# Kernel tuning notes

Measured on AMD Instinct MI355X. Metric: run time of the kernel, lower is better.

Reference implementation:

```python
import jax, jax.numpy as jnp
import numpy as np
from jax import lax

B0, H0, W0, C0, NH0 = 8, 128, 128, 192, 6
SPLIT = (8, 16)
BN_EPS = 1e-5


def setup_inputs() -> dict:
    key = jax.random.key(0)
    ks = jax.random.split(key, 32)
    r = lambda i, shape, s=0.02: jax.random.normal(ks[i], shape, dtype=jnp.float32) * s
    C, C8 = C0, C0 // 8
    L = H0 * W0
    return dict(
        x=jax.random.normal(ks[0], (B0, L, C), dtype=jnp.float32),
        w_qkv=r(1, (C, 3 * C)), b_qkv=r(2, (3 * C,)),
        w_dw1=r(3, (C, 1, 3, 3), 0.1), b_dw1=r(4, (C,)),
        g_bn1=1.0 + r(5, (C,)), be_bn1=r(6, (C,)),
        w_si1=r(7, (C8, C), 0.05), b_si1=r(8, (C8,)),
        g_si=1.0 + r(9, (C8,)), be_si=r(10, (C8,)),
        w_si2=r(11, (1, C8), 0.05), b_si2=r(12, (1,)),
        w_ci1=r(13, (C8, C), 0.05), b_ci1=r(14, (C8,)),
        g_ci=1.0 + r(15, (C8,)), be_ci=r(16, (C8,)),
        w_ci2=r(17, (C, C8), 0.05), b_ci2=r(18, (C,)),
        w_dw2=r(19, (C, 1, 3, 3), 0.1), b_dw2=r(20, (C,)),
        g_bn2=1.0 + r(21, (C,)), be_bn2=r(22, (C,)),
        w_proj=r(23, (C, C)), b_proj=r(24, (C,)),
        H=H0, W=W0,
    )


def _bn(x, g, b):  # eval-mode BatchNorm2d, running_mean=0, running_var=1, NCHW
    return x * (g / jnp.sqrt(1.0 + BN_EPS))[:, None, None] + b[:, None, None]


def _gelu(x):
    return jax.nn.gelu(x, approximate=False)  # torch nn.GELU default (erf)


def _dwconv3x3(x, w, b):  # x:(B,C,H,W), w:(C,1,3,3) depthwise
    y = lax.conv_general_dilated(x, w, (1, 1), 'SAME',
                                 feature_group_count=x.shape[1],
                                 dimension_numbers=('NCHW', 'OIHW', 'NCHW'))
    return y + b[:, None, None]


def _c1x1(x, w, b):  # 1x1 conv, w:(O,C)
    return jnp.einsum('bchw,oc->bohw', x, w) + b[:, None, None]


def _win_attn(q, k, v, H, W, Hs, Ws, nh):
    # q,k,v: (B, H*W, Cb). qkv1==qkv2==qkv3 in the source (same Linear on same x),
    # so attn1+attn2+attn3 == 3*attn1 and v1+v2+v3 == 3*v1 (faithful math).
    B, L, Cb = q.shape
    hd = Cb // nh
    scale = hd ** (-0.5)
    T = Hs * Ws

    def to_win(t):  # (B,L,Cb) -> (nW, nh, T, hd)
        t = t.reshape(B, H // Hs, Hs, W // Ws, Ws, Cb)
        t = t.transpose(0, 1, 3, 2, 4, 5).reshape(-1, T, nh, hd)
        return t.transpose(0, 2, 1, 3)

    qw, kw, vw = to_win(q), to_win(k), to_win(v)
    attn = jnp.einsum('wntd,wnsd->wnts', qw, kw) * (3.0 * scale)
    attn = jax.nn.softmax(attn, axis=-1)
    out = jnp.einsum('wnts,wnsd->wntd', attn, 3.0 * vw)  # (nW, nh, T, hd)
    out = out.transpose(0, 2, 1, 3).reshape(-1, T, Cb)
    out = out.reshape(B, H // Hs, W // Ws, Hs, Ws, Cb)
    out = out.transpose(0, 1, 3, 2, 4, 5).reshape(B, H, W, Cb)
    return out


def _forward(x, w_qkv, b_qkv, w_dw1, b_dw1, g_bn1, be_bn1,
             w_si1, b_si1, g_si, be_si, w_si2, b_si2,
             w_ci1, b_ci1, g_ci, be_ci, w_ci2, b_ci2,
             w_dw2, b_dw2, g_bn2, be_bn2, w_proj, b_proj, H, W):
    B, L, C = x.shape
    Ch = C // 2
    nh = NH0 // 2

    qkv = (x @ w_qkv + b_qkv).reshape(B, L, 3, C).transpose(2, 0, 1, 3)  # (3,B,L,C)
    mx = max(SPLIT)
    pad_b = (mx - H % mx) % mx
    pad_r = (mx - W % mx) % mx
    qi = qkv.reshape(3 * B, H, W, C)
    qi = jnp.pad(qi, ((0, 0), (0, pad_b), (0, pad_r), (0, 0)))
    _H, _W = H + pad_b, W + pad_r
    qkv = qi.reshape(3, B, _H * _W, C)
    q, k, v = qkv[0], qkv[1], qkv[2]

    fu1 = _win_attn(q[..., :Ch], k[..., :Ch], v[..., :Ch], _H, _W, SPLIT[0], SPLIT[1], nh)
    fu2 = _win_attn(q[..., Ch:], k[..., Ch:], v[..., Ch:], _H, _W, SPLIT[1], SPLIT[0], nh)
    fu = jnp.concatenate([fu1[:, :H, :W, :].reshape(B, L, Ch),
                          fu2[:, :H, :W, :].reshape(B, L, Ch)], axis=-1)

    # NOTE: the source does x.reshape(B,C,L) (a raw reshape, NOT a transpose) -- replicated.
    x_img = x.reshape(B, C, H, W)
    conv_x1 = _gelu(_bn(_dwconv3x3(x_img, w_dw1, b_dw1), g_bn1, be_bn1))

    s = _c1x1(conv_x1, w_si1, b_si1)
    s = _c1x1(_gelu(_bn(s, g_si, be_si)), w_si2, b_si2)   # (B,1,H,W)
    spatial_map = s.reshape(B, L, 1)

    c = conv_x1.mean(axis=(2, 3), keepdims=True)           # AdaptiveAvgPool2d(1)
    c = _c1x1(c, w_ci1, b_ci1)
    c = _c1x1(_gelu(_bn(c, g_ci, be_ci)), w_ci2, b_ci2)    # (B,C,1,1)
    channel_map = c.reshape(B, 1, C)

    fu = fu + fu * jax.nn.sigmoid(spatial_map)
    fu_img = jnp.swapaxes(fu, -2, -1).reshape(B, C, H, W)
    fu_img = _gelu(_bn(_dwconv3x3(fu_img, w_dw2, b_dw2), g_bn2, be_bn2))
    fu = fu_img.transpose(0, 2, 3, 1).reshape(B, L, C)
    fu = fu + fu * jax.nn.sigmoid(channel_map)
    return fu @ w_proj + b_proj


def reference(x, w_qkv, b_qkv, w_dw1, b_dw1, g_bn1, be_bn1,
              w_si1, b_si1, g_si, be_si, w_si2, b_si2,
              w_ci1, b_ci1, g_ci, be_ci, w_ci2, b_ci2,
              w_dw2, b_dw2, g_bn2, be_bn2, w_proj, b_proj, H, W):
    return _forward(x, w_qkv, b_qkv, w_dw1, b_dw1, g_bn1, be_bn1,
                    w_si1, b_si1, g_si, be_si, w_si2, b_si2,
                    w_ci1, b_ci1, g_ci, be_ci, w_ci2, b_ci2,
                    w_dw2, b_dw2, g_bn2, be_bn2, w_proj, b_proj, H, W)
```

## Files before the change

### kernel.cpp

```cpp
#include <hip/hip_runtime.h>

#define Bn 8
#define Hn 128
#define Wn 128
#define Cn 192
#define Ln (Hn*Wn)
#define Mn (Bn*Ln)
#define FUn ((size_t)Mn*Cn)
#define BANKn ((size_t)Mn*96)
#define BN_RSQ 0.9999950000374997f

typedef unsigned short ushort_t;
typedef __attribute__((ext_vector_type(8))) short short8;
typedef __attribute__((ext_vector_type(4))) float f32x4;
typedef __attribute__((ext_vector_type(4))) unsigned int uint4v;

static __device__ __forceinline__ float gelu_f(float x) {
    return 0.5f * x * (1.0f + erff(x * 0.7071067811865475f));
}
static __device__ __forceinline__ float gate1p(float x) {
    return 1.0f + 1.0f / (1.0f + __expf(-x));
}
static __device__ __forceinline__ unsigned short f2bf(float f) {
    unsigned u = __float_as_uint(f);
    return (unsigned short)((u + 0x7FFFu + ((u >> 16) & 1u)) >> 16);
}
static __device__ __forceinline__ unsigned int pk2(float lo, float hi) {
    return (unsigned int)f2bf(lo) | ((unsigned int)f2bf(hi) << 16);
}
static __device__ __forceinline__ float bf2f(ushort_t u) {
    return __uint_as_float((unsigned)u << 16);
}

__global__ __launch_bounds__(256) void qkv_mfma(const ushort_t* __restrict__ Ab,
        const float* __restrict__ Bw, const float* __restrict__ bias,
        ushort_t* __restrict__ Qp, ushort_t* __restrict__ Kp,
        ushort_t* __restrict__ Vp)
{
    __shared__ __align__(16) ushort_t As[128 * 64];
    __shared__ __align__(16) ushort_t Bs[96 * 64];
    const int m0 = blockIdx.y * 128;
    const int n0g = blockIdx.x * 96;
    const int part = n0g / 192;
    const int coln = n0g - part * 192;
    ushort_t* dst = part == 0 ? Qp : (part == 1 ? Kp : Vp);
    ushort_t* bptr = dst + (coln ? BANKn : 0);
    const int tid = threadIdx.x;
    const int lane = tid & 63;
    const int wrow = (tid >> 6) * 32;
    const int r0 = lane >> 4, cl = lane & 15;
    f32x4 acc[2][6] = {};

    for (int ks = 0; ks < 3; ++ks) {
        const int k0 = ks * 64;
        if (ks) __syncthreads();
        #pragma unroll
        for (int i = 0; i < 2; ++i) {
            int s = tid + i * 256;
            int row = s >> 2, q = s & 3;
            const ushort_t* src = Ab + (size_t)(m0 + row) * 192 + k0 + q * 16;
            uint4 u0 = *(const uint4*)(src);
            uint4 u1 = *(const uint4*)(src + 8);
            int r7 = row & 7;
            *(uint4*)&As[row * 64 + (((q * 2) ^ r7) * 8)] = u0;
            *(uint4*)&As[row * 64 + (((q * 2 + 1) ^ r7) * 8)] = u1;
        }
        #pragma unroll
        for (int i = 0; i < 3; ++i) {
            int f = tid + i * 256;
            int col = f % 96, kslot = f / 96;
            uint4v wv;
            #pragma unroll
            for (int e2 = 0; e2 < 4; ++e2) {
                float lo = Bw[(size_t)(k0 + kslot * 8 + 2 * e2)     * 576 + n0g + col];
                float hi = Bw[(size_t)(k0 + kslot * 8 + 2 * e2 + 1) * 576 + n0g + col];
                wv[e2] = pk2(lo, hi);
            }
            *(uint4v*)&Bs[col * 64 + ((kslot ^ (col & 7)) * 8)] = wv;
        }
        __syncthreads();
        #pragma unroll
        for (int kk = 0; kk < 2; ++kk) {
            int kslot = kk * 4 + r0;
            int ra0 = wrow + cl, ra1 = wrow + 16 + cl;
            short8 a0 = *(const short8*)&As[ra0 * 64 + ((kslot ^ (ra0 & 7)) * 8)];
            short8 a1 = *(const short8*)&As[ra1 * 64 + ((kslot ^ (ra1 & 7)) * 8)];
            #pragma unroll
            for (int n = 0; n < 6; ++n) {
                int col = n * 16 + cl;
                short8 bn = *(const short8*)&Bs[col * 64 + ((kslot ^ (col & 7)) * 8)];
                acc[0][n] = __builtin_amdgcn_mfma_f32_16x16x32_bf16(a0, bn, acc[0][n], 0, 0, 0);
                acc[1][n] = __builtin_amdgcn_mfma_f32_16x16x32_bf16(a1, bn, acc[1][n], 0, 0, 0);
            }
        }
    }
    float bv[6];
    #pragma unroll
    for (int n = 0; n < 6; ++n) bv[n] = bias[n0g + n * 16 + cl];
    #pragma unroll
    for (int m = 0; m < 2; ++m) {
        #pragma unroll
        for (int j = 0; j < 4; ++j) {
            int row = m0 + wrow + m * 16 + r0 * 4 + j;
            int b = row >> 14, l = row & 16383;
            int h = l >> 7, w = l & 127;
            int win, t;
            if (coln == 0) { win = (h >> 3) * 8 + (w >> 4);  t = (h & 7) * 16 + (w & 15); }
            else           { win = (h >> 4) * 16 + (w >> 3); t = (h & 15) * 8 + (w & 7); }
            size_t rbase = ((size_t)((b * 128 + win) * 128 + t)) * 96;
            #pragma unroll
            for (int n = 0; n < 6; ++n)
                bptr[rbase + n * 16 + cl] = f2bf(acc[m][n][j] + bv[n]);
        }
    }
}

__global__ __launch_bounds__(256) void proj_mfma(const ushort_t* __restrict__ Ab,
        const float* __restrict__ Bw, const float* __restrict__ bias,
        float* __restrict__ Cout)
{
    __shared__ __align__(16) ushort_t As[128 * 64];
    __shared__ __align__(16) ushort_t Bs[96 * 64];
    const int m0 = blockIdx.x * 128;
    const int n0 = blockIdx.y * 96;
    const int tid = threadIdx.x;
    const int lane = tid & 63;
    const int wrow = (tid >> 6) * 32;
    const int r0 = lane >> 4, cl = lane & 15;
    f32x4 acc[2][6] = {};

    for (int ks = 0; ks < 3; ++ks) {
        const int k0 = ks * 64;
        if (ks) __syncthreads();
        #pragma unroll
        for (int i = 0; i < 2; ++i) {
            int s = tid + i * 256;
            int row = s >> 2, q = s & 3;
            const ushort_t* src = Ab + (size_t)(m0 + row) * 192 + k0 + q * 16;
            uint4 u0 = *(const uint4*)(src);
            uint4 u1 = *(const uint4*)(src + 8);
            int r7 = row & 7;
            *(uint4*)&As[row * 64 + (((q * 2) ^ r7) * 8)] = u0;
            *(uint4*)&As[row * 64 + (((q * 2 + 1) ^ r7) * 8)] = u1;
        }
        #pragma unroll
        for (int i = 0; i < 3; ++i) {
            int f = tid + i * 256;
            int col = f % 96, kslot = f / 96;
            uint4v wv;
            #pragma unroll
            for (int e2 = 0; e2 < 4; ++e2) {
                float lo = Bw[(size_t)(k0 + kslot * 8 + 2 * e2)     * 192 + n0 + col];
                float hi = Bw[(size_t)(k0 + kslot * 8 + 2 * e2 + 1) * 192 + n0 + col];
                wv[e2] = pk2(lo, hi);
            }
            *(uint4v*)&Bs[col * 64 + ((kslot ^ (col & 7)) * 8)] = wv;
        }
        __syncthreads();
        #pragma unroll
        for (int kk = 0; kk < 2; ++kk) {
            int kslot = kk * 4 + r0;
            int ra0 = wrow + cl, ra1 = wrow + 16 + cl;
            short8 a0 = *(const short8*)&As[ra0 * 64 + ((kslot ^ (ra0 & 7)) * 8)];
            short8 a1 = *(const short8*)&As[ra1 * 64 + ((kslot ^ (ra1 & 7)) * 8)];
            #pragma unroll
            for (int n = 0; n < 6; ++n) {
                int col = n * 16 + cl;
                short8 bn = *(const short8*)&Bs[col * 64 + ((kslot ^ (col & 7)) * 8)];
                acc[0][n] = __builtin_amdgcn_mfma_f32_16x16x32_bf16(a0, bn, acc[0][n], 0, 0, 0);
                acc[1][n] = __builtin_amdgcn_mfma_f32_16x16x32_bf16(a1, bn, acc[1][n], 0, 0, 0);
            }
        }
    }
    #pragma unroll
    for (int m = 0; m < 2; ++m) {
        #pragma unroll
        for (int n = 0; n < 6; ++n) {
            int col = n0 + n * 16 + cl;
            float bv = bias[col];
            #pragma unroll
            for (int j = 0; j < 4; ++j) {
                int row = m0 + wrow + m * 16 + r0 * 4 + j;
                Cout[(size_t)row * 192 + col] = acc[m][n][j] + bv;
            }
        }
    }
}

__global__ __launch_bounds__(256) void attn_mfma(const ushort_t* __restrict__ Qp,
        const ushort_t* __restrict__ Kp, const ushort_t* __restrict__ Vp,
        const float* __restrict__ gate_s, ushort_t* __restrict__ fu_b)
{
    const int widx = threadIdx.x >> 6;
    const int idx = blockIdx.x * 4 + widx;
    const int jhalf = idx & 1;
    const int sub0 = idx >> 1;
    const int branch = (sub0 >= 3072) ? 1 : 0;
    const int sub = sub0 - branch * 3072;
    const int head = sub >> 10;
    const int b = (sub >> 7) & 7;
    const int win = sub & 127;
    const int L = threadIdx.x & 63;
    const int g = L >> 4, q = L & 15;
    int hb, wb;
    if (branch == 0) { hb = (win >> 3) * 8;  wb = (win & 7) * 16; }
    else             { hb = (win >> 4) * 16; wb = (win & 15) * 8; }
    const int cf = branch * 96 + head * 32;
    const int hch = head * 32;
    const int jbase = jhalf * 4;

    const size_t bank = branch ? BANKn : 0;
    const size_t wbase = ((size_t)((b * 128 + win) * 128)) * 96;
    const ushort_t* Qw = Qp + bank + wbase;
    const ushort_t* Kw = Kp + bank + wbase;
    const ushort_t* Vw = Vp + bank + wbase;

    short8 kf[8], qf[4];
    #pragma unroll
    for (int i = 0; i < 8; ++i)
        kf[i] = *(const short8*)(Kw + (size_t)(16 * i + q) * 96 + hch + 8 * g);
    #pragma unroll
    for (int jj = 0; jj < 4; ++jj)
        qf[jj] = *(const short8*)(Qw + (size_t)(16 * (jbase + jj) + q) * 96 + hch + 8 * g);
    short8 vf[2][4];
    {
        #pragma unroll
        for (int s = 0; s < 4; ++s) {
            #pragma unroll
            for (int dblk = 0; dblk < 2; ++dblk) {
                uint4v wv;
                #pragma unroll
                for (int e2 = 0; e2 < 4; ++e2) {
                    size_t base = (size_t)(32 * s + 8 * g + 2 * e2) * 96 + hch + 16 * dblk + q;
                    unsigned lo = Vw[base];
                    unsigned hi = Vw[base + 96];
                    wv[e2] = lo | (hi << 16);
                }
                vf[dblk][s] = *(short8*)&wv;
            }
        }
    }

    const float SC = 0.5303300858899106f;
    const int src0 = q + ((g & 1) << 5);
    const bool thi = (g >> 1) != 0;
    const bool glo = (g < 2);
    #pragma unroll
    for (int jj = 0; jj < 4; ++jj) {
        const int j = jbase + jj;
        unsigned wA[8], wB[8];
        float ss = 0.0f;
        #pragma unroll
        for (int i = 0; i < 8; ++i) {
            f32x4 z = {};
            f32x4 S = __builtin_amdgcn_mfma_f32_16x16x32_bf16(kf[i], qf[jj], z, 0, 0, 0);
            float p0 = __expf(S[0] * SC), p1 = __expf(S[1] * SC);
            float p2 = __expf(S[2] * SC), p3 = __expf(S[3] * SC);
            ss += (p0 + p1) + (p2 + p3);
            wA[i] = pk2(p0, p1);
            wB[i] = pk2(p2, p3);
        }
        ss += __shfl_xor(ss, 16);
        ss += __shfl_xor(ss, 32);
        int l_own;
        if (branch == 0) l_own = (hb + j) * Wn + wb + q;
        else             l_own = (hb + 2 * j + (q >> 3)) * Wn + wb + (q & 7);
        float s_own = 3.0f * gate_s[(size_t)b * Ln + l_own] / ss;

        f32x4 O0 = {}, O1 = {};
        #pragma unroll
        for (int s = 0; s < 4; ++s) {
            unsigned a0  = (unsigned)__shfl((int)wA[2*s],     src0);
            unsigned b0  = (unsigned)__shfl((int)wB[2*s],     src0);
            unsigned a0h = (unsigned)__shfl((int)wA[2*s],     src0 + 16);
            unsigned b0h = (unsigned)__shfl((int)wB[2*s],     src0 + 16);
            unsigned a1  = (unsigned)__shfl((int)wA[2*s+1],   src0);
            unsigned b1  = (unsigned)__shfl((int)wB[2*s+1],   src0);
            unsigned a1h = (unsigned)__shfl((int)wA[2*s+1],   src0 + 16);
            unsigned b1h = (unsigned)__shfl((int)wB[2*s+1],   src0 + 16);
            uint4v B2u;
            B2u[0] = thi ? a1  : a0;
            B2u[1] = thi ? b1  : b0;
            B2u[2] = thi ? a1h : a0h;
            B2u[3] = thi ? b1h : b0h;
            short8 B2 = *(short8*)&B2u;
            O0 = __builtin_amdgcn_mfma_f32_16x16x32_bf16(vf[0][s], B2, O0, 0, 0, 0);
            O1 = __builtin_amdgcn_mfma_f32_16x16x32_bf16(vf[1][s], B2, O1, 0, 0, 0);
        }
        unsigned w0 = pk2(O0[0] * s_own, O0[1] * s_own);
        unsigned w1 = pk2(O0[2] * s_own, O0[3] * s_own);
        unsigned w2 = pk2(O1[0] * s_own, O1[1] * s_own);
        unsigned w3 = pk2(O1[2] * s_own, O1[3] * s_own);
        unsigned a0 = (unsigned)__shfl((int)w0, src0);
        unsigned a1 = (unsigned)__shfl((int)w1, src0);
        unsigned b0 = (unsigned)__shfl((int)w0, src0 + 16);
        unsigned b1 = (unsigned)__shfl((int)w1, src0 + 16);
        unsigned c0 = (unsigned)__shfl((int)w2, src0);
        unsigned c1 = (unsigned)__shfl((int)w3, src0);
        unsigned d0 = (unsigned)__shfl((int)w2, src0 + 16);
        unsigned d1 = (unsigned)__shfl((int)w3, src0 + 16);
        uint4 o = make_uint4(glo ? a0 : c0, glo ? a1 : c1,
                             glo ? b0 : d0, glo ? b1 : d1);
        *(uint4*)(fu_b + (size_t)(b * Ln + l_own) * 192 + cf + 8 * g) = o;
    }
}

__global__ __launch_bounds__(256) void conv1_k(const float* __restrict__ x,
        const float* __restrict__ wdw, const float* __restrict__ bdw,
        const float* __restrict__ g1, const float* __restrict__ be1,
        ushort_t* __restrict__ conv1b, ushort_t* __restrict__ xb,
        float* __restrict__ pooled2)
{
    int bc = blockIdx.x;
    int half = blockIdx.y;
    int c = bc % 192;
    const float* plane = x + (size_t)bc * Ln;
    ushort_t* oplane = conv1b + (size_t)bc * Ln;
    ushort_t* xplane = xb + (size_t)bc * Ln;
    int t = threadIdx.x;
    int sx = t & 31, sy = t >> 5;
    int w0 = sx * 4, h0 = half * 64 + sy * 8;
    float wk[9];
    #pragma unroll
    for (int i = 0; i < 9; ++i) wk[i] = wdw[c * 9 + i];
    float gb = g1[c] * BN_RSQ, bb = be1[c], bd = bdw[c];

    float r[10][6];
    #pragma unroll
    for (int i = 0; i < 10; ++i) {
        int h = h0 - 1 + i;
        float4 m = make_float4(0.f, 0.f, 0.f, 0.f);
        if (h >= 0 && h < Hn)
            m = *(const float4*)(plane + h * Wn + w0);
        float lf = __shfl_up(m.w, 1);
        float rt = __shfl_down(m.x, 1);
        r[i][0] = sx ? lf : 0.0f;
        r[i][1] = m.x; r[i][2] = m.y; r[i][3] = m.z; r[i][4] = m.w;
        r[i][5] = (sx < 31) ? rt : 0.0f;
    }
    float psum = 0.0f;
    #pragma unroll
    for (int i = 0; i < 8; ++i) {
        int h = h0 + i;
        *(uint2*)(xplane + h * Wn + w0) =
            make_uint2(pk2(r[i+1][1], r[i+1][2]), pk2(r[i+1][3], r[i+1][4]));
        float o[4];
        #pragma unroll
        for (int p = 0; p < 4; ++p) {
            float s = wk[0] * r[i][p];
            s = fmaf(wk[1], r[i][p + 1], s);
            s = fmaf(wk[2], r[i][p + 2], s);
            s = fmaf(wk[3], r[i+1][p],     s);
            s = fmaf(wk[4], r[i+1][p + 1], s);
            s = fmaf(wk[5], r[i+1][p + 2], s);
            s = fmaf(wk[6], r[i+2][p],     s);
            s = fmaf(wk[7], r[i+2][p + 1], s);
            s = fmaf(wk[8], r[i+2][p + 2], s);
            float y = gelu_f((s + bd) * gb + bb);
            psum += y;
            o[p] = y;
        }
        *(uint2*)(oplane + h * Wn + w0) =
            make_uint2(pk2(o[0], o[1]), pk2(o[2], o[3]));
    }
    __shared__ float red[4];
    for (int off = 32; off; off >>= 1) psum += __shfl_down(psum, off);
    if ((t & 63) == 0) red[t >> 6] = psum;
    __syncthreads();
    if (t == 0)
        pooled2[bc * 2 + half] = red[0] + red[1] + red[2] + red[3];
}

__global__ __launch_bounds__(128) void spatial_gate_k(const ushort_t* __restrict__ conv1b,
        const float* __restrict__ ws1g, const float* __restrict__ bs1,
        const float* __restrict__ gsi, const float* __restrict__ besi,
        const float* __restrict__ ws2, const float* __restrict__ bs2,
        float* __restrict__ gate_s)
{
    int bh = blockIdx.x;
    int b = bh >> 7, h = bh & 127;
    int w = threadIdx.x;
    __shared__ float ws1T[192 * 24];
    for (int i = w; i < 192 * 24; i += 128) {
        int c = i / 24, o = i - c * 24;
        ws1T[i] = ws1g[o * 192 + c];
    }
    __syncthreads();
    float acc24[24] = {};
    const ushort_t* base = conv1b + (size_t)b * 192 * Ln + h * Wn + w;
    #pragma unroll 4
    for (int c = 0; c < 192; ++c) {
        float v = bf2f(base[(size_t)c * Ln]);
        const float4* wp = (const float4*)&ws1T[c * 24];
        #pragma unroll
        for (int o4 = 0; o4 < 6; ++o4) {
            float4 wv = wp[o4];
            acc24[o4*4+0] = fmaf(v, wv.x, acc24[o4*4+0]);
            acc24[o4*4+1] = fmaf(v, wv.y, acc24[o4*4+1]);
            acc24[o4*4+2] = fmaf(v, wv.z, acc24[o4*4+2]);
            acc24[o4*4+3] = fmaf(v, wv.w, acc24[o4*4+3]);
        }
    }
    float s2 = bs2[0];
    #pragma unroll
    for (int o = 0; o < 24; ++o)
        s2 = fmaf(gelu_f((acc24[o] + bs1[o]) * (gsi[o] * BN_RSQ) + besi[o]), ws2[o], s2);
    gate_s[(size_t)bh * 128 + w] = gate1p(s2);
}

__global__ __launch_bounds__(192) void channel_gate_k(const float* __restrict__ pooled2,
        const float* __restrict__ w1, const float* __restrict__ b1,
        const float* __restrict__ g, const float* __restrict__ be,
        const float* __restrict__ w2, const float* __restrict__ b2,
        float* __restrict__ gate_c)
{
    int b = blockIdx.x, t = threadIdx.x;
    __shared__ float pl[192];
    __shared__ float h1[24];
    int bc = b * 192 + t;
    pl[t] = (pooled2[bc * 2] + pooled2[bc * 2 + 1]) * (1.0f / Ln);
    __syncthreads();
    if (t < 24) {
        float a = b1[t];
        for (int c = 0; c < 192; ++c) a = fmaf(pl[c], w1[t * 192 + c], a);
        a = a * (g[t] * BN_RSQ) + be[t];
        h1[t] = gelu_f(a);
    }
    __syncthreads();
    float a = b2[t];
    #pragma unroll
    for (int o = 0; o < 24; ++o) a = fmaf(h1[o], w2[t * 24 + o], a);
    gate_c[b * 192 + t] = gate1p(a);
}

__global__ __launch_bounds__(256) void dwconv2_k(const ushort_t* __restrict__ fu_b,
        const float* __restrict__ gate_c,
        const float* __restrict__ wdw, const float* __restrict__ bdw,
        const float* __restrict__ g2, const float* __restrict__ be2,
        ushort_t* __restrict__ out2b)
{
    int bh = blockIdx.x >> 1;
    int whalf = blockIdx.x & 1;
    int b = bh >> 7, h = bh & 127;
    int tid = threadIdx.x;
    __shared__ float cwp[24 * 105];
    for (int idx = tid; idx < 24 * 96; idx += 256) {
        int c8 = idx / 96, r = idx - c8 * 96;
        float v;
        if (r < 72) {
            int i = r / 9, p = r - i * 9;
            v = wdw[(c8 * 8 + i) * 9 + p];
        } else {
            int r2 = r - 72;
            int i = r2 / 3, j = r2 - i * 3;
            int c = c8 * 8 + i;
            float A = g2[c] * BN_RSQ;
            v = (j == 0) ? A : (j == 1) ? fmaf(bdw[c], A, be2[c])
                                        : gate_c[b * 192 + c];
        }
        cwp[c8 * 105 + r] = v;
    }
    __syncthreads();
    const size_t outrow = (size_t)(b * Ln + h * Wn) * 192;
    for (int it = 0; it < 6; ++it) {
        int item = it * 256 + tid;
        int w = whalf * 64 + item / 24;
        int c8 = item % 24;
        int co = c8 * 8;
        const float* wp = &cwp[c8 * 105];
        uint4 nb[3][3];
        #pragma unroll
        for (int r = 0; r < 3; ++r)
            #pragma unroll
            for (int d = 0; d < 3; ++d)
                nb[r][d] = make_uint4(0u, 0u, 0u, 0u);
        #pragma unroll
        for (int r = 0; r < 3; ++r) {
            int hh = h - 1 + r;
            if (hh < 0 || hh >= Hn) continue;
            const ushort_t* rp = fu_b + (size_t)(b * Ln + hh * Wn) * 192 + co;
            #pragma unroll
            for (int d = 0; d < 3; ++d) {
                int w2 = w - 1 + d;
                if (w2 < 0 || w2 >= Wn) continue;
                nb[r][d] = *(const uint4*)(rp + (size_t)w2 * 192);
            }
        }
        unsigned ou[4];
        #pragma unroll
        for (int i = 0; i < 8; ++i) {
            float s = 0.0f;
            #pragma unroll
            for (int r = 0; r < 3; ++r) {
                #pragma unroll
                for (int d = 0; d < 3; ++d) {
                    unsigned word = ((const unsigned*)&nb[r][d])[i >> 1];
                    float v = __uint_as_float((i & 1) ? (word & 0xffff0000u)
                                                      : (word << 16));
                    s = fmaf(wp[i * 9 + r * 3 + d], v, s);
                }
            }
            float A = wp[72 + i * 3];
            float Bc = wp[72 + i * 3 + 1];
            float G = wp[72 + i * 3 + 2];
            float y = gelu_f(fmaf(s, A, Bc)) * G;
            if (i & 1) ou[i >> 1] |= (unsigned)f2bf(y) << 16;
            else       ou[i >> 1] = (unsigned)f2bf(y);
        }
        *(uint4*)(out2b + outrow + (size_t)w * 192 + co) =
            make_uint4(ou[0], ou[1], ou[2], ou[3]);
    }
}

extern "C" void kernel_launch(void* const* d_in, const int* in_sizes, int n_in,
                              void* d_out, int out_size, void* d_ws, size_t ws_size,
                              hipStream_t stream) {
    (void)in_sizes; (void)n_in; (void)out_size; (void)ws_size;
    const float* x      = (const float*)d_in[0];
    const float* w_qkv  = (const float*)d_in[1];
    const float* b_qkv  = (const float*)d_in[2];
    const float* w_dw1  = (const float*)d_in[3];
    const float* b_dw1  = (const float*)d_in[4];
    const float* g_bn1  = (const float*)d_in[5];
    const float* be_bn1 = (const float*)d_in[6];
    const float* w_si1  = (const float*)d_in[7];
    const float* b_si1  = (const float*)d_in[8];
    const float* g_si   = (const float*)d_in[9];
    const float* be_si  = (const float*)d_in[10];
    const float* w_si2  = (const float*)d_in[11];
    const float* b_si2  = (const float*)d_in[12];
    const float* w_ci1  = (const float*)d_in[13];
    const float* b_ci1  = (const float*)d_in[14];
    const float* g_ci   = (const float*)d_in[15];
    const float* be_ci  = (const float*)d_in[16];
    const float* w_ci2  = (const float*)d_in[17];
    const float* b_ci2  = (const float*)d_in[18];
    const float* w_dw2  = (const float*)d_in[19];
    const float* b_dw2  = (const float*)d_in[20];
    const float* g_bn2  = (const float*)d_in[21];
    const float* be_bn2 = (const float*)d_in[22];
    const float* w_proj = (const float*)d_in[23];
    const float* b_proj = (const float*)d_in[24];

    float* ws = (float*)d_ws;
    ushort_t* conv1b = (ushort_t*)ws;
    ushort_t* Qp     = (ushort_t*)ws;
    ushort_t* Kp     = (ushort_t*)(ws + FUn / 2);
    ushort_t* out2b  = (ushort_t*)(ws + 8000000);
    float* gate_s    = ws + FUn;
    float* gate_c    = gate_s + (size_t)Bn * Ln;
    float* pooled2   = gate_c + Bn * 192;
    ushort_t* xb     = (ushort_t*)d_out;
    ushort_t* fu_b   = (ushort_t*)d_out;
    ushort_t* Vp     = (ushort_t*)d_out + FUn;

    conv1_k<<<dim3(Bn * 192, 2), 256, 0, stream>>>(x, w_dw1, b_dw1, g_bn1, be_bn1,
                                                   conv1b, xb, pooled2);
    spatial_gate_k<<<Bn * Hn, 128, 0, stream>>>(conv1b, w_si1, b_si1, g_si, be_si,
                                                w_si2, b_si2, gate_s);
    channel_gate_k<<<Bn, 192, 0, stream>>>(pooled2, w_ci1, b_ci1, g_ci, be_ci,
                                           w_ci2, b_ci2, gate_c);
    qkv_mfma<<<dim3(6, Mn / 128), 256, 0, stream>>>(xb, w_qkv, b_qkv, Qp, Kp, Vp);
    attn_mfma<<<3072, 256, 0, stream>>>(Qp, Kp, Vp, gate_s, fu_b);
    dwconv2_k<<<Bn * Hn * 2, 256, 0, stream>>>(fu_b, gate_c,
                                               w_dw2, b_dw2, g_bn2, be_bn2, out2b);
    proj_mfma<<<dim3(Mn / 128, 2), 256, 0, stream>>>(out2b, w_proj, b_proj, (float*)d_out);
}
```

Baseline: 310.5 us.

## Store Q/K/V per-head contiguous with transposed V; split conv1 into more blocks

The QKV GEMM epilogue now writes each window/head as a contiguous 128x32 tile, with V stored transposed (channel-major), so the attention kernel loads K, Q and V fragments as vector short8 loads instead of strided scalar gathers. Separately, conv1 is split into 16 row groups per plane, one row per thread, so it launches more blocks and reloads fewer halo rows per thread, with 16 partial pooled sums reduced in channel_gate. The scattered 2-byte epilogue stores in the QKV kernel may become less coalesced, and conv1 re-reads two halo rows per output row.

```diff
diff --git a/kernel.cpp b/kernel.cpp
--- a/kernel.cpp
+++ b/kernel.cpp
@@ -107,10 +107,15 @@
             int win, t;
             if (coln == 0) { win = (h >> 3) * 8 + (w >> 4);  t = (h & 7) * 16 + (w & 15); }
             else           { win = (h >> 4) * 16 + (w >> 3); t = (h & 15) * 8 + (w & 7); }
-            size_t rbase = ((size_t)((b * 128 + win) * 128 + t)) * 96;
-            #pragma unroll
-            for (int n = 0; n < 6; ++n)
-                bptr[rbase + n * 16 + cl] = f2bf(acc[m][n][j] + bv[n]);
+            size_t wb3 = (size_t)(b * 128 + win) * 3;
+            #pragma unroll
+            for (int n = 0; n < 6; ++n) {
+                int col96 = n * 16 + cl;
+                int head = col96 >> 5, ch = col96 & 31;
+                size_t off = (wb3 + head) * 4096 +
+                             (part == 2 ? ch * 128 + t : t * 32 + ch);
+                bptr[off] = f2bf(acc[m][n][j] + bv[n]);
+            }
         }
     }
 }
@@ -206,40 +211,27 @@
     if (branch == 0) { hb = (win >> 3) * 8;  wb = (win & 7) * 16; }
     else             { hb = (win >> 4) * 16; wb = (win & 15) * 8; }
     const int cf = branch * 96 + head * 32;
-    const int hch = head * 32;
     const int jbase = jhalf * 4;
 
-    const size_t bank = branch ? BANKn : 0;
-    const size_t wbase = ((size_t)((b * 128 + win) * 128)) * 96;
-    const ushort_t* Qw = Qp + bank + wbase;
-    const ushort_t* Kw = Kp + bank + wbase;
-    const ushort_t* Vw = Vp + bank + wbase;
+    const size_t base = (branch ? BANKn : 0)
+                      + ((size_t)(b * 128 + win) * 3 + head) * 4096;
+    const ushort_t* Qw = Qp + base;
+    const ushort_t* Kw = Kp + base;
+    const ushort_t* Vw = Vp + base;
 
     short8 kf[8], qf[4];
     #pragma unroll
     for (int i = 0; i < 8; ++i)
-        kf[i] = *(const short8*)(Kw + (size_t)(16 * i + q) * 96 + hch + 8 * g);
+        kf[i] = *(const short8*)(Kw + (16 * i + q) * 32 + 8 * g);
     #pragma unroll
     for (int jj = 0; jj < 4; ++jj)
-        qf[jj] = *(const short8*)(Qw + (size_t)(16 * (jbase + jj) + q) * 96 + hch + 8 * g);
+        qf[jj] = *(const short8*)(Qw + (16 * (jbase + jj) + q) * 32 + 8 * g);
     short8 vf[2][4];
-    {
-        #pragma unroll
-        for (int s = 0; s < 4; ++s) {
-            #pragma unroll
-            for (int dblk = 0; dblk < 2; ++dblk) {
-                uint4v wv;
-                #pragma unroll
-                for (int e2 = 0; e2 < 4; ++e2) {
-                    size_t base = (size_t)(32 * s + 8 * g + 2 * e2) * 96 + hch + 16 * dblk + q;
-                    unsigned lo = Vw[base];
-                    unsigned hi = Vw[base + 96];
-                    wv[e2] = lo | (hi << 16);
-                }
-                vf[dblk][s] = *(short8*)&wv;
-            }
-        }
-    }
+    #pragma unroll
+    for (int dblk = 0; dblk < 2; ++dblk)
+        #pragma unroll
+        for (int s = 0; s < 4; ++s)
+            vf[dblk][s] = *(const short8*)(Vw + (16 * dblk + q) * 128 + 32 * s + 8 * g);
 
     const float SC = 0.5303300858899106f;
     const int src0 = q + ((g & 1) << 5);
@@ -309,66 +301,60 @@
         const float* __restrict__ wdw, const float* __restrict__ bdw,
         const float* __restrict__ g1, const float* __restrict__ be1,
         ushort_t* __restrict__ conv1b, ushort_t* __restrict__ xb,
-        float* __restrict__ pooled2)
+        float* __restrict__ pooled16)
 {
     int bc = blockIdx.x;
-    int half = blockIdx.y;
+    int rg = blockIdx.y;
     int c = bc % 192;
     const float* plane = x + (size_t)bc * Ln;
-    ushort_t* oplane = conv1b + (size_t)bc * Ln;
-    ushort_t* xplane = xb + (size_t)bc * Ln;
     int t = threadIdx.x;
     int sx = t & 31, sy = t >> 5;
-    int w0 = sx * 4, h0 = half * 64 + sy * 8;
+    int w0 = sx * 4, h = rg * 8 + sy;
     float wk[9];
     #pragma unroll
     for (int i = 0; i < 9; ++i) wk[i] = wdw[c * 9 + i];
     float gb = g1[c] * BN_RSQ, bb = be1[c], bd = bdw[c];
 
-    float r[10][6];
-    #pragma unroll
-    for (int i = 0; i < 10; ++i) {
-        int h = h0 - 1 + i;
+    float a[3][6];
+    #pragma unroll
+    for (int i = 0; i < 3; ++i) {
+        int hh = h - 1 + i;
         float4 m = make_float4(0.f, 0.f, 0.f, 0.f);
-        if (h >= 0 && h < Hn)
-            m = *(const float4*)(plane + h * Wn + w0);
+        if (hh >= 0 && hh < Hn)
+            m = *(const float4*)(plane + hh * Wn + w0);
         float lf = __shfl_up(m.w, 1);
         float rt = __shfl_down(m.x, 1);
-        r[i][0] = sx ? lf : 0.0f;
-        r[i][1] = m.x; r[i][2] = m.y; r[i][3] = m.z; r[i][4] = m.w;
-        r[i][5] = (sx < 31) ? rt : 0.0f;
-    }
+        a[i][0] = sx ? lf : 0.0f;
+        a[i][1] = m.x; a[i][2] = m.y; a[i][3] = m.z; a[i][4] = m.w;
+        a[i][5] = (sx < 31) ? rt : 0.0f;
+    }
+    *(uint2*)(xb + (size_t)bc * Ln + h * Wn + w0) =
+        make_uint2(pk2(a[1][1], a[1][2]), pk2(a[1][3], a[1][4]));
     float psum = 0.0f;
-    #pragma unroll
-    for (int i = 0; i < 8; ++i) {
-        int h = h0 + i;
-        *(uint2*)(xplane + h * Wn + w0) =
-            make_uint2(pk2(r[i+1][1], r[i+1][2]), pk2(r[i+1][3], r[i+1][4]));
-        float o[4];
-        #pragma unroll
-        for (int p = 0; p < 4; ++p) {
-            float s = wk[0] * r[i][p];
-            s = fmaf(wk[1], r[i][p + 1], s);
-            s = fmaf(wk[2], r[i][p + 2], s);
-            s = fmaf(wk[3], r[i+1][p],     s);
-            s = fmaf(wk[4], r[i+1][p + 1], s);
-            s = fmaf(wk[5], r[i+1][p + 2], s);
-            s = fmaf(wk[6], r[i+2][p],     s);
-            s = fmaf(wk[7], r[i+2][p + 1], s);
-            s = fmaf(wk[8], r[i+2][p + 2], s);
-            float y = gelu_f((s + bd) * gb + bb);
-            psum += y;
-            o[p] = y;
-        }
-        *(uint2*)(oplane + h * Wn + w0) =
-            make_uint2(pk2(o[0], o[1]), pk2(o[2], o[3]));
-    }
+    float o[4];
+    #pragma unroll
+    for (int p = 0; p < 4; ++p) {
+        float s = wk[0] * a[0][p];
+        s = fmaf(wk[1], a[0][p + 1], s);
+        s = fmaf(wk[2], a[0][p + 2], s);
+        s = fmaf(wk[3], a[1][p],     s);
+        s = fmaf(wk[4], a[1][p + 1], s);
+        s = fmaf(wk[5], a[1][p + 2], s);
+        s = fmaf(wk[6], a[2][p],     s);
+        s = fmaf(wk[7], a[2][p + 1], s);
+        s = fmaf(wk[8], a[2][p + 2], s);
+        float y = gelu_f((s + bd) * gb + bb);
+        psum += y;
+        o[p] = y;
+    }
+    *(uint2*)(conv1b + (size_t)bc * Ln + h * Wn + w0) =
+        make_uint2(pk2(o[0], o[1]), pk2(o[2], o[3]));
     __shared__ float red[4];
     for (int off = 32; off; off >>= 1) psum += __shfl_down(psum, off);
     if ((t & 63) == 0) red[t >> 6] = psum;
     __syncthreads();
     if (t == 0)
-        pooled2[bc * 2 + half] = red[0] + red[1] + red[2] + red[3];
+        pooled16[bc * 16 + rg] = red[0] + red[1] + red[2] + red[3];
 }
 
 __global__ __launch_bounds__(128) void spatial_gate_k(const ushort_t* __restrict__ conv1b,
@@ -408,7 +394,7 @@
     gate_s[(size_t)bh * 128 + w] = gate1p(s2);
 }
 
-__global__ __launch_bounds__(192) void channel_gate_k(const float* __restrict__ pooled2,
+__global__ __launch_bounds__(192) void channel_gate_k(const float* __restrict__ pooled16,
         const float* __restrict__ w1, const float* __restrict__ b1,
         const float* __restrict__ g, const float* __restrict__ be,
         const float* __restrict__ w2, const float* __restrict__ b2,
@@ -418,7 +404,10 @@
     __shared__ float pl[192];
     __shared__ float h1[24];
     int bc = b * 192 + t;
-    pl[t] = (pooled2[bc * 2] + pooled2[bc * 2 + 1]) * (1.0f / Ln);
+    float s = 0.0f;
+    #pragma unroll
+    for (int i = 0; i < 16; ++i) s += pooled16[bc * 16 + i];
+    pl[t] = s * (1.0f / Ln);
     __syncthreads();
     if (t < 24) {
         float a = b1[t];
@@ -549,16 +538,16 @@
     ushort_t* out2b  = (ushort_t*)(ws + 8000000);
     float* gate_s    = ws + FUn;
     float* gate_c    = gate_s + (size_t)Bn * Ln;
-    float* pooled2   = gate_c + Bn * 192;
+    float* pooled16  = gate_c + Bn * 192;
     ushort_t* xb     = (ushort_t*)d_out;
     ushort_t* fu_b   = (ushort_t*)d_out;
     ushort_t* Vp     = (ushort_t*)d_out + FUn;
 
-    conv1_k<<<dim3(Bn * 192, 2), 256, 0, stream>>>(x, w_dw1, b_dw1, g_bn1, be_bn1,
-                                                   conv1b, xb, pooled2);
+    conv1_k<<<dim3(Bn * 192, 16), 256, 0, stream>>>(x, w_dw1, b_dw1, g_bn1, be_bn1,
+                                                    conv1b, xb, pooled16);
     spatial_gate_k<<<Bn * Hn, 128, 0, stream>>>(conv1b, w_si1, b_si1, g_si, be_si,
                                                 w_si2, b_si2, gate_s);
-    channel_gate_k<<<Bn, 192, 0, stream>>>(pooled2, w_ci1, b_ci1, g_ci, be_ci,
+    channel_gate_k<<<Bn, 192, 0, stream>>>(pooled16, w_ci1, b_ci1, g_ci, be_ci,
                                            w_ci2, b_ci2, gate_c);
     qkv_mfma<<<dim3(6, Mn / 128), 256, 0, stream>>>(xb, w_qkv, b_qkv, Qp, Kp, Vp);
     attn_mfma<<<3072, 256, 0, stream>>>(Qp, Kp, Vp, gate_s, fu_b);
```

Result: slower. 340.4 us (+9.6%).
